# Performance work log

Hardware: AMD Instinct MI355X
Metric: run time of the kernel (lower is better)

The kernel has to match this reference:

```python
import jax, jax.numpy as jnp
import numpy as np

STATE_LEN = 256
EPS = 1e-5


def _ln(x, g, b):
    m = jnp.mean(x, axis=-1, keepdims=True)
    v = jnp.mean((x - m) ** 2, axis=-1, keepdims=True)
    return (x - m) / jnp.sqrt(v + EPS) * g + b


def setup_inputs() -> dict:
    key = jax.random.key(0)
    ks = jax.random.split(key, 12)
    B, S, L, D, DK, DV = 2, 256, 2048, 512, 64, 64
    T = L + 2 * S  # 2560
    def w(k, i, o):
        return jax.random.normal(k, (i, o), jnp.float32) * 0.02
    return {
        "x": jax.random.normal(ks[0], (B, T, D), jnp.float32),
        "w_q": w(ks[1], D, DK), "w_k": w(ks[2], D, DK), "w_v": w(ks[3], D, DV),
        "w_q_ss": w(ks[4], D, DK), "w_k_ss": w(ks[5], D, DK), "w_v_ss": w(ks[6], D, DV),
        "w_q_se": w(ks[7], D, DK), "w_k_se": w(ks[8], D, DK), "w_v_se": w(ks[9], D, DV),
        "ln_g": jnp.ones((D,), jnp.float32), "ln_b": jnp.zeros((D,), jnp.float32),
        "ln_g_ss": jnp.ones((D,), jnp.float32), "ln_b_ss": jnp.zeros((D,), jnp.float32),
        "ln_g_se": jnp.ones((D,), jnp.float32), "ln_b_se": jnp.zeros((D,), jnp.float32),
        "cope_emb": jax.random.normal(ks[10], (1, DK, T), jnp.float32),
    }


def reference(x, w_q, w_k, w_v, w_q_ss, w_k_ss, w_v_ss, w_q_se, w_k_se, w_v_se,
              ln_g, ln_b, ln_g_ss, ln_b_ss, ln_g_se, ln_b_se, cope_emb):
    S = STATE_LEN
    T = x.shape[1]
    # extract_state: [state_start | main | state_end]
    xs, xm, xe = x[:, :S], x[:, S:T - S], x[:, T - S:]
    xm = _ln(xm, ln_g, ln_b)
    xs = _ln(xs, ln_g_ss, ln_b_ss)
    xe = _ln(xe, ln_g_se, ln_b_se)
    q = jnp.concatenate([xs @ w_q_ss, xm @ w_q, xe @ w_q_se], axis=1)  # [B,T,DK]
    k = jnp.concatenate([xs @ w_k_ss, xm @ w_k, xe @ w_k_se], axis=1)
    v = jnp.concatenate([xs @ w_v_ss, xm @ w_v, xe @ w_v_se], axis=1)
    dk = q.shape[-1]
    # --- CoPE bias ---
    logits = jnp.einsum('btd,bsd->bts', q, k)  # [B,T,T]
    gates = jax.nn.sigmoid(logits)
    # reverse cumsum along keys (flip-cumsum-flip)
    pos = jnp.flip(jnp.cumsum(jnp.flip(gates, -1), axis=-1), -1)
    pos = jnp.minimum(pos, jnp.float32(T - 1))
    pf = jnp.floor(pos)
    pc = jnp.ceil(pos)
    li = jnp.einsum('btd,dm->btm', q, cope_emb[0])  # [B,T,T]
    lc = jnp.take_along_axis(li, pc.astype(jnp.int32), axis=-1)
    lf = jnp.take_along_axis(li, pf.astype(jnp.int32), axis=-1)
    w = pos - pf
    bias = lc * w + lf * (1.0 - w)
    # --- attention with tril-log mask + CoPE bias ---
    causal = jnp.tril(jnp.ones((T, T), dtype=bool))
    att_logits = logits / jnp.sqrt(jnp.float32(dk)) + jnp.where(causal, bias, -jnp.inf)
    attn = jax.nn.softmax(att_logits, axis=-1)
    return jnp.einsum('bts,bsd->btd', attn, v)
```

## Files before the change

### kernel.cpp

```cpp
#include <hip/hip_runtime.h>
#include <hip/hip_bf16.h>
#include <math.h>

using short8 = __attribute__((ext_vector_type(8))) short;
using f32x4  = __attribute__((ext_vector_type(4))) float;

constexpr int S_LEN  = 256;
constexpr int T      = 2560;
constexpr int D_IN   = 512;
constexpr int DK     = 64;
constexpr int B_N    = 2;
constexpr int SS     = 16;

__global__ __launch_bounds__(256) void ln_kernel(
    const float* __restrict__ x,
    const float* __restrict__ g_m,  const float* __restrict__ b_m,
    const float* __restrict__ g_s,  const float* __restrict__ b_s,
    const float* __restrict__ g_e,  const float* __restrict__ b_e,
    __hip_bfloat16* __restrict__ xnh, __hip_bfloat16* __restrict__ xnl)
{
    const int wv   = threadIdx.x >> 6;
    const int lane = threadIdx.x & 63;
    const int row  = blockIdx.x * 4 + wv;
    const int t    = row % T;

    const float *gv, *bv;
    if (t < S_LEN)          { gv = g_s; bv = b_s; }
    else if (t < T - S_LEN) { gv = g_m; bv = b_m; }
    else                    { gv = g_e; bv = b_e; }

    const float4* xr4 = (const float4*)(x + (size_t)row * D_IN);
    float4 a = xr4[lane * 2], b4 = xr4[lane * 2 + 1];
    float xv[8] = {a.x, a.y, a.z, a.w, b4.x, b4.y, b4.z, b4.w};

    float s = 0.f;
#pragma unroll
    for (int j = 0; j < 8; ++j) s += xv[j];
#pragma unroll
    for (int off = 32; off > 0; off >>= 1) s += __shfl_down(s, off);
    s = __shfl(s, 0);
    const float mean = s * (1.0f / D_IN);

    float sq = 0.f;
#pragma unroll
    for (int j = 0; j < 8; ++j) { float d = xv[j] - mean; sq += d * d; }
#pragma unroll
    for (int off = 32; off > 0; off >>= 1) sq += __shfl_down(sq, off);
    sq = __shfl(sq, 0);
    const float inv = rsqrtf(sq * (1.0f / D_IN) + 1e-5f);

    const float4* gv4 = (const float4*)gv;
    const float4* bv4 = (const float4*)bv;
    float4 ga = gv4[lane * 2], gb = gv4[lane * 2 + 1];
    float4 ba = bv4[lane * 2], bb = bv4[lane * 2 + 1];
    float g8[8] = {ga.x, ga.y, ga.z, ga.w, gb.x, gb.y, gb.z, gb.w};
    float b8[8] = {ba.x, ba.y, ba.z, ba.w, bb.x, bb.y, bb.z, bb.w};

    short hs[8], ls[8];
#pragma unroll
    for (int j = 0; j < 8; ++j) {
        float v = (xv[j] - mean) * inv * g8[j] + b8[j];
        __hip_bfloat16 h  = __float2bfloat16(v);
        __hip_bfloat16 lo = __float2bfloat16(v - __bfloat162float(h));
        hs[j] = *(short*)&h;
        ls[j] = *(short*)&lo;
    }
    short8 H = {hs[0],hs[1],hs[2],hs[3],hs[4],hs[5],hs[6],hs[7]};
    short8 L = {ls[0],ls[1],ls[2],ls[3],ls[4],ls[5],ls[6],ls[7]};
    *(short8*)(xnh + (size_t)row * D_IN + lane * 8) = H;
    *(short8*)(xnl + (size_t)row * D_IN + lane * 8) = L;
}

__global__ __launch_bounds__(256) void prep_kernel(
    const float* __restrict__ w_qs, const float* __restrict__ w_ks, const float* __restrict__ w_vs,
    const float* __restrict__ w_q,  const float* __restrict__ w_k,  const float* __restrict__ w_v,
    const float* __restrict__ w_qe, const float* __restrict__ w_ke, const float* __restrict__ w_ve,
    const float* __restrict__ cope,
    __hip_bfloat16* __restrict__ wth, __hip_bfloat16* __restrict__ wtl,
    __hip_bfloat16* __restrict__ copeT)
{
    const int i = blockIdx.x * 256 + threadIdx.x;
    constexpr int NW = 9 * DK * D_IN;
    if (i < NW) {
        const int matIdx = i >> 15;
        const int rem = i & 32767;
        const int col = rem >> 9, k = rem & 511;
        const float* W =
            (matIdx == 0) ? w_qs : (matIdx == 1) ? w_ks : (matIdx == 2) ? w_vs :
            (matIdx == 3) ? w_q  : (matIdx == 4) ? w_k  : (matIdx == 5) ? w_v  :
            (matIdx == 6) ? w_qe : (matIdx == 7) ? w_ke : w_ve;
        float f = W[(size_t)k * DK + col];
        __hip_bfloat16 h = __float2bfloat16(f);
        wth[i] = h;
        wtl[i] = __float2bfloat16(f - __bfloat162float(h));
    } else {
        const int j = i - NW;
        const int m = j >> 6, d = j & 63;
        copeT[j] = __float2bfloat16(cope[(size_t)d * T + m]);
    }
}

__global__ __launch_bounds__(256) void qkv_gemm_kernel(
    const __hip_bfloat16* __restrict__ xnh, const __hip_bfloat16* __restrict__ xnl,
    const __hip_bfloat16* __restrict__ wth, const __hip_bfloat16* __restrict__ wtl,
    __hip_bfloat16* __restrict__ qh, __hip_bfloat16* __restrict__ ql,
    __hip_bfloat16* __restrict__ kh, __hip_bfloat16* __restrict__ kl,
    __hip_bfloat16* __restrict__ vT)
{
    const int bid = blockIdx.x;
    const int mt = bid / 3, mat = bid % 3;
    const int r0 = mt * 64;
    const int b  = r0 / T, t0 = r0 % T;
    const int region = (t0 < S_LEN) ? 0 : (t0 < T - S_LEN) ? 1 : 2;
    const int matIdx = region * 3 + mat;

    const int tid = threadIdx.x, lane = tid & 63, wid = tid >> 6;
    const int wm = wid >> 1, wn = wid & 1;
    const int fr = lane & 15, k8 = (lane >> 4) * 8;

    f32x4 acc[2][2];
#pragma unroll
    for (int mf = 0; mf < 2; ++mf)
#pragma unroll
        for (int nf = 0; nf < 2; ++nf) acc[mf][nf] = (f32x4){0.f, 0.f, 0.f, 0.f};

    for (int ks = 0; ks < D_IN / 32; ++ks) {
        const int k = ks * 32 + k8;
        short8 ah[2], al[2], bh2[2], bl2[2];
#pragma unroll
        for (int mf = 0; mf < 2; ++mf) {
            size_t off = (size_t)(r0 + wm * 32 + mf * 16 + fr) * D_IN + k;
            ah[mf] = *(const short8*)(xnh + off);
            al[mf] = *(const short8*)(xnl + off);
        }
#pragma unroll
        for (int nf = 0; nf < 2; ++nf) {
            size_t off = ((size_t)matIdx * DK + wn * 32 + nf * 16 + fr) * D_IN + k;
            bh2[nf] = *(const short8*)(wth + off);
            bl2[nf] = *(const short8*)(wtl + off);
        }
#pragma unroll
        for (int mf = 0; mf < 2; ++mf)
#pragma unroll
            for (int nf = 0; nf < 2; ++nf) {
                acc[mf][nf] = __builtin_amdgcn_mfma_f32_16x16x32_bf16(ah[mf], bh2[nf], acc[mf][nf], 0, 0, 0);
                acc[mf][nf] = __builtin_amdgcn_mfma_f32_16x16x32_bf16(ah[mf], bl2[nf], acc[mf][nf], 0, 0, 0);
                acc[mf][nf] = __builtin_amdgcn_mfma_f32_16x16x32_bf16(al[mf], bh2[nf], acc[mf][nf], 0, 0, 0);
            }
    }

    const int r4 = (lane >> 4) * 4;
#pragma unroll
    for (int mf = 0; mf < 2; ++mf)
#pragma unroll
        for (int nf = 0; nf < 2; ++nf) {
            const int cg = wn * 32 + nf * 16 + fr;
#pragma unroll
            for (int j = 0; j < 4; ++j) {
                const int rg = r0 + wm * 32 + mf * 16 + r4 + j;
                float f = acc[mf][nf][j];
                __hip_bfloat16 h  = __float2bfloat16(f);
                __hip_bfloat16 lo = __float2bfloat16(f - __bfloat162float(h));
                if (mat == 0)      { qh[(size_t)rg * DK + cg] = h; ql[(size_t)rg * DK + cg] = lo; }
                else if (mat == 1) { kh[(size_t)rg * DK + cg] = h; kl[(size_t)rg * DK + cg] = lo; }
                else               { vT[((size_t)b * DK + cg) * T + (rg % T)] = h; }
            }
        }
}

__global__ __launch_bounds__(256) void gemm1_kernel(
    const __hip_bfloat16* __restrict__ qh, const __hip_bfloat16* __restrict__ ql,
    const __hip_bfloat16* __restrict__ kh, const __hip_bfloat16* __restrict__ kl,
    const __hip_bfloat16* __restrict__ copeT,
    float* __restrict__ logc, __hip_bfloat16* __restrict__ lic,
    int b0, int t_off, int TC)
{
    constexpr int TS = T / 64;
    const int per_b = (TC / 128) * TS;
    const int bb  = blockIdx.x / per_b;
    const int rem = blockIdx.x % per_b;
    const int ti  = rem / TS, si = rem % TS;
    const int t0  = ti * 128, s0 = si * 64;
    const int b   = b0 + bb;
    float*          logits_c = logc + (size_t)bb * TC * T;
    __hip_bfloat16* li_c     = lic  + (size_t)bb * TC * T;

    const int tid = threadIdx.x, lane = tid & 63, wid = tid >> 6;
    const int wm  = wid >> 1, wn = wid & 1;
    const int fr  = lane & 15, k8 = (lane >> 4) * 8;
    const size_t qb = (size_t)b * T * DK;

    short8 ah[4][2], al[4][2];
#pragma unroll
    for (int mf = 0; mf < 4; ++mf)
#pragma unroll
        for (int ks = 0; ks < 2; ++ks) {
            size_t off = qb + (size_t)(t_off + t0 + wm * 64 + mf * 16 + fr) * DK + ks * 32 + k8;
            ah[mf][ks] = *(const short8*)(qh + off);
            al[mf][ks] = *(const short8*)(ql + off);
        }
    short8 bh[2][2], bl[2][2], bc[2][2];
#pragma unroll
    for (int nf = 0; nf < 2; ++nf)
#pragma unroll
        for (int ks = 0; ks < 2; ++ks) {
            size_t off = (size_t)(s0 + wn * 32 + nf * 16 + fr) * DK + ks * 32 + k8;
            bh[nf][ks] = *(const short8*)(kh + qb + off);
            bl[nf][ks] = *(const short8*)(kl + qb + off);
            bc[nf][ks] = *(const short8*)(copeT + off);
        }

    f32x4 accL[4][2], accM[4][2];
#pragma unroll
    for (int mf = 0; mf < 4; ++mf)
#pragma unroll
        for (int nf = 0; nf < 2; ++nf) {
            accL[mf][nf] = (f32x4){0.f, 0.f, 0.f, 0.f};
            accM[mf][nf] = (f32x4){0.f, 0.f, 0.f, 0.f};
        }

#pragma unroll
    for (int mf = 0; mf < 4; ++mf)
#pragma unroll
        for (int nf = 0; nf < 2; ++nf)
#pragma unroll
            for (int ks = 0; ks < 2; ++ks) {
                accL[mf][nf] = __builtin_amdgcn_mfma_f32_16x16x32_bf16(ah[mf][ks], bh[nf][ks], accL[mf][nf], 0, 0, 0);
                accL[mf][nf] = __builtin_amdgcn_mfma_f32_16x16x32_bf16(ah[mf][ks], bl[nf][ks], accL[mf][nf], 0, 0, 0);
                accL[mf][nf] = __builtin_amdgcn_mfma_f32_16x16x32_bf16(al[mf][ks], bh[nf][ks], accL[mf][nf], 0, 0, 0);
                accM[mf][nf] = __builtin_amdgcn_mfma_f32_16x16x32_bf16(ah[mf][ks], bc[nf][ks], accM[mf][nf], 0, 0, 0);
            }

    const int r4 = (lane >> 4) * 4;
#pragma unroll
    for (int mf = 0; mf < 4; ++mf)
#pragma unroll
        for (int nf = 0; nf < 2; ++nf) {
            const int cg = s0 + wn * 32 + nf * 16 + fr;
#pragma unroll
            for (int j = 0; j < 4; ++j) {
                const int rl = t0 + wm * 64 + mf * 16 + r4 + j;
                const size_t o = (size_t)rl * T + cg;
                logits_c[o] = accL[mf][nf][j];
                li_c[o]     = __float2bfloat16(accM[mf][nf][j]);
            }
        }
}

__global__ __launch_bounds__(256) void phase2_kernel(
    float* __restrict__ logc, const __hip_bfloat16* __restrict__ lic,
    int t_off, int TC)
{
    constexpr int CH = T / 256;
    const int tid  = threadIdx.x;
    const int lane = tid & 63;
    const int wv   = tid >> 6;
    const int bb   = blockIdx.x / TC;
    const int rl   = blockIdx.x % TC;
    const int t    = t_off + rl;

    __shared__ __hip_bfloat16 sli[T];
    __shared__ float redS[4], redM[4], redE[4];

    float*                lrow  = logc + ((size_t)bb * TC + rl) * T;
    const __hip_bfloat16* lirow = lic  + ((size_t)bb * TC + rl) * T;

#pragma unroll
    for (int i = 0; i < 5; ++i) {
        const int idx = i * 256 + tid;
        ((unsigned int*)sli)[idx] = ((const unsigned int*)lirow)[idx];
    }

    const int s0 = tid * CH;
    float lg[CH], g[CH];
    float lsum = 0.f;
    const float2* lr2 = (const float2*)(lrow + s0);
#pragma unroll
    for (int i = 0; i < 5; ++i) {
        float2 v = lr2[i];
        lg[2 * i] = v.x; lg[2 * i + 1] = v.y;
    }
#pragma unroll
    for (int i = 0; i < CH; ++i) {
        g[i] = 1.0f / (1.0f + __expf(-lg[i]));
        lsum += g[i];
    }

    float incl = lsum;
#pragma unroll
    for (int off = 1; off < 64; off <<= 1) {
        float n = __shfl_up(incl, off);
        if (lane >= off) incl += n;
    }
    if (lane == 63) redS[wv] = incl;
    __syncthreads();
    float total = 0.f, wpre = 0.f;
#pragma unroll
    for (int w2 = 0; w2 < 4; ++w2) {
        float tw = redS[w2];
        total += tw;
        if (w2 < wv) wpre += tw;
    }
    float run = wpre + incl - lsum;

    float att[CH];
    float lmax = -INFINITY;
#pragma unroll
    for (int i = 0; i < CH; ++i) {
        int s = s0 + i;
        float pos = total - run;
        run += g[i];
        pos = fminf(pos, (float)(T - 1));
        float pf = floorf(pos);
        float w  = pos - pf;
        int ipf  = (int)pf;
        int ipc  = (int)ceilf(pos);
        float bias = __bfloat162float(sli[ipc]) * w
                   + __bfloat162float(sli[ipf]) * (1.0f - w);
        float al = lg[i] * 0.125f + bias;
        if (s > t) al = -INFINITY;
        att[i] = al;
        lmax = fmaxf(lmax, al);
    }

#pragma unroll
    for (int off = 32; off > 0; off >>= 1) lmax = fmaxf(lmax, __shfl_down(lmax, off));
    if (lane == 0) redM[wv] = lmax;
    __syncthreads();
    const float bmax = fmaxf(fmaxf(redM[0], redM[1]), fmaxf(redM[2], redM[3]));

    float e[CH];
    float esum = 0.f;
#pragma unroll
    for (int i = 0; i < CH; ++i) {
        e[i] = __expf(att[i] - bmax);
        esum += e[i];
    }
#pragma unroll
    for (int off = 32; off > 0; off >>= 1) esum += __shfl_down(esum, off);
    if (lane == 0) redE[wv] = esum;
    __syncthreads();
    const float rden = 1.0f / (redE[0] + redE[1] + redE[2] + redE[3]);

    float2* pw = (float2*)(lrow + s0);
#pragma unroll
    for (int i = 0; i < 5; ++i)
        pw[i] = make_float2(e[2 * i] * rden, e[2 * i + 1] * rden);
}

__global__ __launch_bounds__(256) void gemm2_kernel(
    const float* __restrict__ logc, const __hip_bfloat16* __restrict__ vT,
    float* __restrict__ part, int b0, int t_off, int TC)
{
    const int per_b = (TC / 128) * SS;
    const int bb  = blockIdx.x / per_b;
    const int rem = blockIdx.x % per_b;
    const int ti  = rem / SS, sc = rem % SS;
    const int t0  = ti * 128;
    const int sb  = sc * (T / SS);
    if (sb > t_off + t0 + 127) return;
    const int b   = b0 + bb;
    const float* p_c = logc + (size_t)bb * TC * T;

    const int tid = threadIdx.x, lane = tid & 63, wid = tid >> 6;
    const int wm  = wid >> 1, wn = wid & 1;
    const int fr  = lane & 15, k8 = (lane >> 4) * 8;
    const size_t vb = (size_t)b * DK * T;

    f32x4 acc[4][2];
#pragma unroll
    for (int mf = 0; mf < 4; ++mf)
#pragma unroll
        for (int nf = 0; nf < 2; ++nf) acc[mf][nf] = (f32x4){0.f, 0.f, 0.f, 0.f};

    for (int ks = 0; ks < (T / SS) / 32; ++ks) {
        const int s = sb + ks * 32 + k8;
        short8 a_h[4], a_l[4], bv[2];
#pragma unroll
        for (int mf = 0; mf < 4; ++mf) {
            const float* pp = p_c + (size_t)(t0 + wm * 64 + mf * 16 + fr) * T + s;
            short hh[8], ll[8];
#pragma unroll
            for (int j = 0; j < 8; ++j) {
                float p = pp[j];
                __hip_bfloat16 h  = __float2bfloat16(p);
                __hip_bfloat16 lo = __float2bfloat16(p - __bfloat162float(h));
                hh[j] = *(short*)&h;
                ll[j] = *(short*)&lo;
            }
            a_h[mf] = (short8){hh[0],hh[1],hh[2],hh[3],hh[4],hh[5],hh[6],hh[7]};
            a_l[mf] = (short8){ll[0],ll[1],ll[2],ll[3],ll[4],ll[5],ll[6],ll[7]};
        }
#pragma unroll
        for (int nf = 0; nf < 2; ++nf)
            bv[nf] = *(const short8*)(vT + vb + (size_t)(wn * 32 + nf * 16 + fr) * T + s);
#pragma unroll
        for (int mf = 0; mf < 4; ++mf)
#pragma unroll
            for (int nf = 0; nf < 2; ++nf) {
                acc[mf][nf] = __builtin_amdgcn_mfma_f32_16x16x32_bf16(a_h[mf], bv[nf], acc[mf][nf], 0, 0, 0);
                acc[mf][nf] = __builtin_amdgcn_mfma_f32_16x16x32_bf16(a_l[mf], bv[nf], acc[mf][nf], 0, 0, 0);
            }
    }

    const int r4 = (lane >> 4) * 4;
#pragma unroll
    for (int mf = 0; mf < 4; ++mf)
#pragma unroll
        for (int nf = 0; nf < 2; ++nf) {
            const int cg = wn * 32 + nf * 16 + fr;
#pragma unroll
            for (int j = 0; j < 4; ++j) {
                const int rl = t0 + wm * 64 + mf * 16 + r4 + j;
                part[(((size_t)bb * SS + sc) * TC + rl) * DK + cg] = acc[mf][nf][j];
            }
        }
}

__global__ __launch_bounds__(256) void reduce_kernel(
    const float* __restrict__ part, float* __restrict__ out,
    int b0, int t_off, int TC)
{
    const int per_b = (TC * DK) / 256;
    const int bb = blockIdx.x / per_b;
    const int ii = (blockIdx.x % per_b) * 256 + threadIdx.x;
    const int rl = ii >> 6, d = ii & 63;
    const int t  = t_off + rl;
    const int sc_max = min(SS - 1, t / (T / SS));
    float s = 0.f;
    for (int sc = 0; sc <= sc_max; ++sc)
        s += part[(((size_t)bb * SS + sc) * TC + rl) * DK + d];
    out[((size_t)(b0 + bb) * T + t) * DK + d] = s;
}

extern "C" void kernel_launch(void* const* d_in, const int* in_sizes, int n_in,
                              void* d_out, int out_size, void* d_ws, size_t ws_size,
                              hipStream_t stream)
{
    const float* x    = (const float*)d_in[0];
    const float* w_q  = (const float*)d_in[1];
    const float* w_k  = (const float*)d_in[2];
    const float* w_v  = (const float*)d_in[3];
    const float* w_qs = (const float*)d_in[4];
    const float* w_ks = (const float*)d_in[5];
    const float* w_vs = (const float*)d_in[6];
    const float* w_qe = (const float*)d_in[7];
    const float* w_ke = (const float*)d_in[8];
    const float* w_ve = (const float*)d_in[9];
    const float* g_m  = (const float*)d_in[10];
    const float* b_m  = (const float*)d_in[11];
    const float* g_s  = (const float*)d_in[12];
    const float* b_s  = (const float*)d_in[13];
    const float* g_e  = (const float*)d_in[14];
    const float* b_e  = (const float*)d_in[15];
    const float* cope = (const float*)d_in[16];

    const size_t n_qk  = (size_t)B_N * T * DK;
    const size_t n_xn  = (size_t)B_N * T * D_IN;
    const size_t n_wt  = (size_t)9 * DK * D_IN;
    const size_t fixedB = 5 * n_qk * 2 + (size_t)T * DK * 2
                        + 2 * n_xn * 2 + 2 * n_wt * 2;
    auto chunkB = [&](size_t TC) -> size_t {
        return TC * (size_t)T * 4
             + TC * (size_t)T * 2
             + (size_t)SS * TC * DK * 4;
    };
    int TC, NB;
    if (fixedB + 2 * chunkB(T) <= ws_size)       { TC = T;    NB = 2; }
    else if (fixedB + chunkB(T) <= ws_size)      { TC = T;    NB = 1; }
    else if (fixedB + chunkB(1280) <= ws_size)   { TC = 1280; NB = 1; }
    else                                         { TC = 640;  NB = 1; }

    char* w = (char*)d_ws;
    __hip_bfloat16* qh    = (__hip_bfloat16*)w; w += n_qk * 2;
    __hip_bfloat16* ql    = (__hip_bfloat16*)w; w += n_qk * 2;
    __hip_bfloat16* kh    = (__hip_bfloat16*)w; w += n_qk * 2;
    __hip_bfloat16* kl    = (__hip_bfloat16*)w; w += n_qk * 2;
    __hip_bfloat16* vT    = (__hip_bfloat16*)w; w += n_qk * 2;
    __hip_bfloat16* copeT = (__hip_bfloat16*)w; w += (size_t)T * DK * 2;
    __hip_bfloat16* xnh   = (__hip_bfloat16*)w; w += n_xn * 2;
    __hip_bfloat16* xnl   = (__hip_bfloat16*)w; w += n_xn * 2;
    __hip_bfloat16* wth   = (__hip_bfloat16*)w; w += n_wt * 2;
    __hip_bfloat16* wtl   = (__hip_bfloat16*)w; w += n_wt * 2;
    float*          logc  = (float*)w;          w += (size_t)NB * TC * T * 4;
    __hip_bfloat16* lic   = (__hip_bfloat16*)w; w += (size_t)NB * TC * T * 2;
    float*          part  = (float*)w;

    ln_kernel<<<(B_N * T) / 4, 256, 0, stream>>>(
        x, g_m, b_m, g_s, b_s, g_e, b_e, xnh, xnl);

    prep_kernel<<<(int)((n_wt + (size_t)T * DK) / 256), 256, 0, stream>>>(
        w_qs, w_ks, w_vs, w_q, w_k, w_v, w_qe, w_ke, w_ve, cope,
        wth, wtl, copeT);

    qkv_gemm_kernel<<<(B_N * T / 64) * 3, 256, 0, stream>>>(
        xnh, xnl, wth, wtl, qh, ql, kh, kl, vT);

    for (int b0 = 0; b0 < B_N; b0 += NB)
        for (int t_off = 0; t_off < T; t_off += TC) {
            gemm1_kernel<<<NB * (TC / 128) * (T / 64), 256, 0, stream>>>(
                qh, ql, kh, kl, copeT, logc, lic, b0, t_off, TC);
            phase2_kernel<<<NB * TC, 256, 0, stream>>>(
                logc, lic, t_off, TC);
            gemm2_kernel<<<NB * (TC / 128) * SS, 256, 0, stream>>>(
                logc, vT, part, b0, t_off, TC);
            reduce_kernel<<<NB * (TC * DK) / 256, 256, 0, stream>>>(
                part, (float*)d_out, b0, t_off, TC);
        }
}
```

Baseline: 116.3 us.

## Store softmax probs as bf16, drop split-precision PV, merge LN/prep, halve split-K

Phase2 now writes the normalized attention probabilities as single bf16 into the li buffer instead of fp32 back into the logits buffer. gemm2 loads them directly as bf16 fragments and issues one MFMA per tile rather than a hi/lo pair, cutting traffic, conversion work and MFMA count. The LayerNorm and weight-prep kernels are merged into one launch, and the split-K factor for the PV GEMM drops from 16 to 8. Probability precision falls from roughly fp32 (hi+lo bf16) to plain bf16, which may affect accuracy.

```diff
diff --git a/kernel.cpp b/kernel.cpp
--- a/kernel.cpp
+++ b/kernel.cpp
@@ -10,76 +10,77 @@
 constexpr int D_IN   = 512;
 constexpr int DK     = 64;
 constexpr int B_N    = 2;
-constexpr int SS     = 16;
-
-__global__ __launch_bounds__(256) void ln_kernel(
+constexpr int SS     = 8;
+
+__global__ __launch_bounds__(256) void lnprep_kernel(
     const float* __restrict__ x,
     const float* __restrict__ g_m,  const float* __restrict__ b_m,
     const float* __restrict__ g_s,  const float* __restrict__ b_s,
     const float* __restrict__ g_e,  const float* __restrict__ b_e,
-    __hip_bfloat16* __restrict__ xnh, __hip_bfloat16* __restrict__ xnl)
-{
-    const int wv   = threadIdx.x >> 6;
-    const int lane = threadIdx.x & 63;
-    const int row  = blockIdx.x * 4 + wv;
-    const int t    = row % T;
-
-    const float *gv, *bv;
-    if (t < S_LEN)          { gv = g_s; bv = b_s; }
-    else if (t < T - S_LEN) { gv = g_m; bv = b_m; }
-    else                    { gv = g_e; bv = b_e; }
-
-    const float4* xr4 = (const float4*)(x + (size_t)row * D_IN);
-    float4 a = xr4[lane * 2], b4 = xr4[lane * 2 + 1];
-    float xv[8] = {a.x, a.y, a.z, a.w, b4.x, b4.y, b4.z, b4.w};
-
-    float s = 0.f;
-#pragma unroll
-    for (int j = 0; j < 8; ++j) s += xv[j];
-#pragma unroll
-    for (int off = 32; off > 0; off >>= 1) s += __shfl_down(s, off);
-    s = __shfl(s, 0);
-    const float mean = s * (1.0f / D_IN);
-
-    float sq = 0.f;
-#pragma unroll
-    for (int j = 0; j < 8; ++j) { float d = xv[j] - mean; sq += d * d; }
-#pragma unroll
-    for (int off = 32; off > 0; off >>= 1) sq += __shfl_down(sq, off);
-    sq = __shfl(sq, 0);
-    const float inv = rsqrtf(sq * (1.0f / D_IN) + 1e-5f);
-
-    const float4* gv4 = (const float4*)gv;
-    const float4* bv4 = (const float4*)bv;
-    float4 ga = gv4[lane * 2], gb = gv4[lane * 2 + 1];
-    float4 ba = bv4[lane * 2], bb = bv4[lane * 2 + 1];
-    float g8[8] = {ga.x, ga.y, ga.z, ga.w, gb.x, gb.y, gb.z, gb.w};
-    float b8[8] = {ba.x, ba.y, ba.z, ba.w, bb.x, bb.y, bb.z, bb.w};
-
-    short hs[8], ls[8];
-#pragma unroll
-    for (int j = 0; j < 8; ++j) {
-        float v = (xv[j] - mean) * inv * g8[j] + b8[j];
-        __hip_bfloat16 h  = __float2bfloat16(v);
-        __hip_bfloat16 lo = __float2bfloat16(v - __bfloat162float(h));
-        hs[j] = *(short*)&h;
-        ls[j] = *(short*)&lo;
-    }
-    short8 H = {hs[0],hs[1],hs[2],hs[3],hs[4],hs[5],hs[6],hs[7]};
-    short8 L = {ls[0],ls[1],ls[2],ls[3],ls[4],ls[5],ls[6],ls[7]};
-    *(short8*)(xnh + (size_t)row * D_IN + lane * 8) = H;
-    *(short8*)(xnl + (size_t)row * D_IN + lane * 8) = L;
-}
-
-__global__ __launch_bounds__(256) void prep_kernel(
     const float* __restrict__ w_qs, const float* __restrict__ w_ks, const float* __restrict__ w_vs,
     const float* __restrict__ w_q,  const float* __restrict__ w_k,  const float* __restrict__ w_v,
     const float* __restrict__ w_qe, const float* __restrict__ w_ke, const float* __restrict__ w_ve,
     const float* __restrict__ cope,
+    __hip_bfloat16* __restrict__ xnh, __hip_bfloat16* __restrict__ xnl,
     __hip_bfloat16* __restrict__ wth, __hip_bfloat16* __restrict__ wtl,
     __hip_bfloat16* __restrict__ copeT)
 {
-    const int i = blockIdx.x * 256 + threadIdx.x;
+    constexpr int LN_BLOCKS = (B_N * T) / 4;
+    if (blockIdx.x < LN_BLOCKS) {
+        const int wv   = threadIdx.x >> 6;
+        const int lane = threadIdx.x & 63;
+        const int row  = blockIdx.x * 4 + wv;
+        const int t    = row % T;
+
+        const float *gv, *bv;
+        if (t < S_LEN)          { gv = g_s; bv = b_s; }
+        else if (t < T - S_LEN) { gv = g_m; bv = b_m; }
+        else                    { gv = g_e; bv = b_e; }
+
+        const float4* xr4 = (const float4*)(x + (size_t)row * D_IN);
+        float4 a = xr4[lane * 2], b4 = xr4[lane * 2 + 1];
+        float xv[8] = {a.x, a.y, a.z, a.w, b4.x, b4.y, b4.z, b4.w};
+
+        float s = 0.f;
+#pragma unroll
+        for (int j = 0; j < 8; ++j) s += xv[j];
+#pragma unroll
+        for (int off = 32; off > 0; off >>= 1) s += __shfl_down(s, off);
+        s = __shfl(s, 0);
+        const float mean = s * (1.0f / D_IN);
+
+        float sq = 0.f;
+#pragma unroll
+        for (int j = 0; j < 8; ++j) { float d = xv[j] - mean; sq += d * d; }
+#pragma unroll
+        for (int off = 32; off > 0; off >>= 1) sq += __shfl_down(sq, off);
+        sq = __shfl(sq, 0);
+        const float inv = rsqrtf(sq * (1.0f / D_IN) + 1e-5f);
+
+        const float4* gv4 = (const float4*)gv;
+        const float4* bv4 = (const float4*)bv;
+        float4 ga = gv4[lane * 2], gb = gv4[lane * 2 + 1];
+        float4 ba = bv4[lane * 2], bb = bv4[lane * 2 + 1];
+        float g8[8] = {ga.x, ga.y, ga.z, ga.w, gb.x, gb.y, gb.z, gb.w};
+        float b8[8] = {ba.x, ba.y, ba.z, ba.w, bb.x, bb.y, bb.z, bb.w};
+
+        short hs[8], ls[8];
+#pragma unroll
+        for (int j = 0; j < 8; ++j) {
+            float v = (xv[j] - mean) * inv * g8[j] + b8[j];
+            __hip_bfloat16 h  = __float2bfloat16(v);
+            __hip_bfloat16 lo = __float2bfloat16(v - __bfloat162float(h));
+            hs[j] = *(short*)&h;
+            ls[j] = *(short*)&lo;
+        }
+        short8 H = {hs[0],hs[1],hs[2],hs[3],hs[4],hs[5],hs[6],hs[7]};
+        short8 L = {ls[0],ls[1],ls[2],ls[3],ls[4],ls[5],ls[6],ls[7]};
+        *(short8*)(xnh + (size_t)row * D_IN + lane * 8) = H;
+        *(short8*)(xnl + (size_t)row * D_IN + lane * 8) = L;
+        return;
+    }
+
+    const int i = (blockIdx.x - LN_BLOCKS) * 256 + threadIdx.x;
     constexpr int NW = 9 * DK * D_IN;
     if (i < NW) {
         const int matIdx = i >> 15;
@@ -93,7 +94,7 @@
         __hip_bfloat16 h = __float2bfloat16(f);
         wth[i] = h;
         wtl[i] = __float2bfloat16(f - __bfloat162float(h));
-    } else {
+    } else if (i < NW + T * DK) {
         const int j = i - NW;
         const int m = j >> 6, d = j & 63;
         copeT[j] = __float2bfloat16(cope[(size_t)d * T + m]);
@@ -248,7 +249,7 @@
 }
 
 __global__ __launch_bounds__(256) void phase2_kernel(
-    float* __restrict__ logc, const __hip_bfloat16* __restrict__ lic,
+    const float* __restrict__ logc, __hip_bfloat16* __restrict__ lic,
     int t_off, int TC)
 {
     constexpr int CH = T / 256;
@@ -262,8 +263,8 @@
     __shared__ __hip_bfloat16 sli[T];
     __shared__ float redS[4], redM[4], redE[4];
 
-    float*                lrow  = logc + ((size_t)bb * TC + rl) * T;
-    const __hip_bfloat16* lirow = lic  + ((size_t)bb * TC + rl) * T;
+    const float*    lrow  = logc + ((size_t)bb * TC + rl) * T;
+    __hip_bfloat16* lirow = lic  + ((size_t)bb * TC + rl) * T;
 
 #pragma unroll
     for (int i = 0; i < 5; ++i) {
@@ -342,14 +343,21 @@
     __syncthreads();
     const float rden = 1.0f / (redE[0] + redE[1] + redE[2] + redE[3]);
 
-    float2* pw = (float2*)(lrow + s0);
-#pragma unroll
-    for (int i = 0; i < 5; ++i)
-        pw[i] = make_float2(e[2 * i] * rden, e[2 * i + 1] * rden);
+    unsigned int pw[5];
+#pragma unroll
+    for (int i = 0; i < 5; ++i) {
+        __hip_bfloat16 p0 = __float2bfloat16(e[2 * i] * rden);
+        __hip_bfloat16 p1 = __float2bfloat16(e[2 * i + 1] * rden);
+        pw[i] = (unsigned int)*(unsigned short*)&p0
+              | ((unsigned int)*(unsigned short*)&p1 << 16);
+    }
+    unsigned int* dst = (unsigned int*)(lirow + s0);
+#pragma unroll
+    for (int i = 0; i < 5; ++i) dst[i] = pw[i];
 }
 
 __global__ __launch_bounds__(256) void gemm2_kernel(
-    const float* __restrict__ logc, const __hip_bfloat16* __restrict__ vT,
+    const __hip_bfloat16* __restrict__ lic, const __hip_bfloat16* __restrict__ vT,
     float* __restrict__ part, int b0, int t_off, int TC)
 {
     const int per_b = (TC / 128) * SS;
@@ -360,7 +368,7 @@
     const int sb  = sc * (T / SS);
     if (sb > t_off + t0 + 127) return;
     const int b   = b0 + bb;
-    const float* p_c = logc + (size_t)bb * TC * T;
+    const __hip_bfloat16* p_c = lic + (size_t)bb * TC * T;
 
     const int tid = threadIdx.x, lane = tid & 63, wid = tid >> 6;
     const int wm  = wid >> 1, wn = wid & 1;
@@ -375,32 +383,18 @@
 
     for (int ks = 0; ks < (T / SS) / 32; ++ks) {
         const int s = sb + ks * 32 + k8;
-        short8 a_h[4], a_l[4], bv[2];
-#pragma unroll
-        for (int mf = 0; mf < 4; ++mf) {
-            const float* pp = p_c + (size_t)(t0 + wm * 64 + mf * 16 + fr) * T + s;
-            short hh[8], ll[8];
-#pragma unroll
-            for (int j = 0; j < 8; ++j) {
-                float p = pp[j];
-                __hip_bfloat16 h  = __float2bfloat16(p);
-                __hip_bfloat16 lo = __float2bfloat16(p - __bfloat162float(h));
-                hh[j] = *(short*)&h;
-                ll[j] = *(short*)&lo;
-            }
-            a_h[mf] = (short8){hh[0],hh[1],hh[2],hh[3],hh[4],hh[5],hh[6],hh[7]};
-            a_l[mf] = (short8){ll[0],ll[1],ll[2],ll[3],ll[4],ll[5],ll[6],ll[7]};
-        }
+        short8 a_p[4], bv[2];
+#pragma unroll
+        for (int mf = 0; mf < 4; ++mf)
+            a_p[mf] = *(const short8*)(p_c + (size_t)(t0 + wm * 64 + mf * 16 + fr) * T + s);
 #pragma unroll
         for (int nf = 0; nf < 2; ++nf)
             bv[nf] = *(const short8*)(vT + vb + (size_t)(wn * 32 + nf * 16 + fr) * T + s);
 #pragma unroll
         for (int mf = 0; mf < 4; ++mf)
 #pragma unroll
-            for (int nf = 0; nf < 2; ++nf) {
-                acc[mf][nf] = __builtin_amdgcn_mfma_f32_16x16x32_bf16(a_h[mf], bv[nf], acc[mf][nf], 0, 0, 0);
-                acc[mf][nf] = __builtin_amdgcn_mfma_f32_16x16x32_bf16(a_l[mf], bv[nf], acc[mf][nf], 0, 0, 0);
-            }
+            for (int nf = 0; nf < 2; ++nf)
+                acc[mf][nf] = __builtin_amdgcn_mfma_f32_16x16x32_bf16(a_p[mf], bv[nf], acc[mf][nf], 0, 0, 0);
     }
 
     const int r4 = (lane >> 4) * 4;
@@ -486,12 +480,12 @@
     __hip_bfloat16* lic   = (__hip_bfloat16*)w; w += (size_t)NB * TC * T * 2;
     float*          part  = (float*)w;
 
-    ln_kernel<<<(B_N * T) / 4, 256, 0, stream>>>(
-        x, g_m, b_m, g_s, b_s, g_e, b_e, xnh, xnl);
-
-    prep_kernel<<<(int)((n_wt + (size_t)T * DK) / 256), 256, 0, stream>>>(
+    constexpr int LN_BLOCKS   = (B_N * T) / 4;
+    const int     PREP_BLOCKS = (int)((n_wt + (size_t)T * DK + 255) / 256);
+    lnprep_kernel<<<LN_BLOCKS + PREP_BLOCKS, 256, 0, stream>>>(
+        x, g_m, b_m, g_s, b_s, g_e, b_e,
         w_qs, w_ks, w_vs, w_q, w_k, w_v, w_qe, w_ke, w_ve, cope,
-        wth, wtl, copeT);
+        xnh, xnl, wth, wtl, copeT);
 
     qkv_gemm_kernel<<<(B_N * T / 64) * 3, 256, 0, stream>>>(
         xnh, xnl, wth, wtl, qh, ql, kh, kl, vT);
@@ -503,7 +497,7 @@
             phase2_kernel<<<NB * TC, 256, 0, stream>>>(
                 logc, lic, t_off, TC);
             gemm2_kernel<<<NB * (TC / 128) * SS, 256, 0, stream>>>(
-                logc, vT, part, b0, t_off, TC);
+                lic, vT, part, b0, t_off, TC);
             reduce_kernel<<<NB * (TC * DK) / 256, 256, 0, stream>>>(
                 part, (float*)d_out, b0, t_off, TC);
         }
```

Measured after the change: 105.6 us. 1.1x faster.
